# Kernel optimization log

Hardware: AMD Instinct MI355X
Metric: run time of the kernel (lower is better)

## Reference

```python
import jax, jax.numpy as jnp
import numpy as np

WS = 8       # window size
HEADS = 2    # num_heads hardcoded in CFPT's Swin_transformer blocks


def _to_windows(t, ws):
    # t: [B, H, W, C] -> [B*nWin, ws*ws, C]
    B, H, W, C = t.shape
    t = t.reshape(B, H // ws, ws, W // ws, ws, C)
    t = t.transpose(0, 1, 3, 2, 4, 5)
    return t.reshape(-1, ws * ws, C)


def _from_windows(t, B, H, W, ws):
    # t: [B*nWin, ws*ws, C] -> [B, H, W, C]
    C = t.shape[-1]
    t = t.reshape(B, H // ws, W // ws, ws, ws, C)
    t = t.transpose(0, 1, 3, 2, 4, 5)
    return t.reshape(B, H, W, C)


def swin_cross_attn(x, y, Wq, Wk, Wv, Wo):
    # Windowed cross-attention: queries from x, keys/values from y.
    # x, y: [B, C, H, W]; Wq/Wk/Wv/Wo: [C, C] (bias-free, no position embedding).
    B, C, H, W = x.shape
    dh = C // HEADS
    xw = _to_windows(x.transpose(0, 2, 3, 1), WS)   # [Bn, T, C], T = WS*WS
    yw = _to_windows(y.transpose(0, 2, 3, 1), WS)
    q = jnp.einsum('btc,dc->btd', xw, Wq)
    k = jnp.einsum('btc,dc->btd', yw, Wk)
    v = jnp.einsum('btc,dc->btd', yw, Wv)
    Bn, T, _ = q.shape
    q = q.reshape(Bn, T, HEADS, dh)
    k = k.reshape(Bn, T, HEADS, dh)
    v = v.reshape(Bn, T, HEADS, dh)
    scale = jnp.asarray(dh, x.dtype) ** -0.5
    scores = jnp.einsum('bqhd,bkhd->bhqk', q, k) * scale   # [Bn, H, T, T]
    attn = jax.nn.softmax(scores, axis=-1)
    o = jnp.einsum('bhqk,bkhd->bqhd', attn, v).reshape(Bn, T, C)
    o = jnp.einsum('btc,dc->btd', o, Wo)
    return _from_windows(o, B, H, W, WS).transpose(0, 3, 1, 2)  # [B, C, H, W]


def setup_inputs() -> dict:
    key = jax.random.key(0)
    ks = jax.random.split(key, 6)
    C = 256
    shapes = [(4, C, 128, 128), (4, C, 64, 64), (4, C, 32, 32), (4, C, 16, 16)]
    feats = [jax.random.normal(ks[i], s, jnp.float32) for i, s in enumerate(shapes)]
    w1 = jax.random.normal(ks[4], (4, 4, C, C), jnp.float32) * 0.02
    w2 = jax.random.normal(ks[5], (4, 4, C, C), jnp.float32) * 0.02
    return {"feat0": feats[0], "feat1": feats[1], "feat2": feats[2],
            "feat3": feats[3], "w1": w1, "w2": w2}


def reference(feat0, feat1, feat2, feat3, w1, w2):
    feats = [feat0, feat1, feat2, feat3]
    l = feats[0].shape[0] // 2
    outs = []
    for i, f in enumerate(feats):
        f1, f2 = f[:l], f[l:]
        # sequential cross-update, as in the original loop body
        f1 = jax.nn.relu(f1 + swin_cross_attn(f1, f2, w1[i, 0], w1[i, 1], w1[i, 2], w1[i, 3]))
        f2 = jax.nn.relu(f2 + swin_cross_attn(f2, f1, w2[i, 0], w2[i, 1], w2[i, 2], w2[i, 3]))
        outs.append(jnp.concatenate([f1, f2], axis=0))
    return tuple(outs)
```

## Files before the change

### kernel.cpp

```cpp
#include <hip/hip_runtime.h>


using bf16x8 = __attribute__((ext_vector_type(8))) __bf16;
using f32x4  = __attribute__((ext_vector_type(4))) float;
using u16x4  = __attribute__((ext_vector_type(4))) unsigned short;
using u16x8  = __attribute__((ext_vector_type(8))) unsigned short;

__device__ __forceinline__ unsigned short f2bf(float f){
  unsigned int x = __float_as_uint(f);
  x += 0x7FFFu + ((x >> 16) & 1u);
  return (unsigned short)(x >> 16);
}
__device__ __forceinline__ float bf2f(unsigned short u){
  return __uint_as_float((unsigned int)u << 16);
}
__device__ __forceinline__ void store_bf4(unsigned short* dst, f32x4 v){
  u16x4 o;
  o[0]=f2bf(v[0]); o[1]=f2bf(v[1]); o[2]=f2bf(v[2]); o[3]=f2bf(v[3]);
  *reinterpret_cast<u16x4*>(dst) = o;
}

#define MFMA16 __builtin_amdgcn_mfma_f32_16x16x32_bf16

__global__ void wcvt_kernel(const float* __restrict__ w1,
// ... 23 lines not shown
  int hw64 = (int)(HW >> 6);
  int bat = r / (4 * hw64);
  int r2 = r - bat * 4 * hw64;
  int ct = r2 / hw64, hwt = r2 - ct * hw64;

  const float* src = feat + (size_t)bat * HW * 256 + (size_t)(ct * 64) * HW + (size_t)hwt * 64;
  int tid = threadIdx.x;
  int cq = tid >> 4, hw0 = (tid & 15) * 4;
  #pragma unroll
  for (int p = 0; p < 4; ++p){
    int c = p * 16 + cq;
    const float* sp = src + (size_t)c * HW + hw0;
    float4 v = *reinterpret_cast<const float4*>(sp);
    T[c][hw0] = v.x; T[c][hw0+1] = v.y; T[c][hw0+2] = v.z; T[c][hw0+3] = v.w;
  }
  __syncthreads();
  unsigned short* dst = Ft + (tbase + (size_t)bat * HW + (size_t)hwt * 64) * 256 + ct * 64;
  #pragma unroll
  for (int p = 0; p < 2; ++p){
    int id = p * 256 + tid;
    int t = id >> 3, c0 = (id & 7) * 8;
    u16x8 o;
    #pragma unroll
    for (int j = 0; j < 8; ++j) o[j] = f2bf(T[c0 + j][t]);
    *reinterpret_cast<u16x8*>(dst + (size_t)t * 256 + c0) = o;
  }
}

__global__ __launch_bounds__(256, 2) void untrans_kernel(
    const unsigned short* __restrict__ Gt, float* __restrict__ outb)
{
  __shared__ float T[64][65];
  int bid = blockIdx.x;
  int r; int Hl; size_t tbase, ooff;
  if (bid < 4096){ r = bid;        Hl = 128; tbase = 0;     ooff = 0; }
  else if (bid < 5120){ r = bid - 4096; Hl = 64; tbase = 65536; ooff = 16777216; }
  else if (bid < 5376){ r = bid - 5120; Hl = 32; tbase = 81920; ooff = 20971520; }
  else { r = bid - 5376; Hl = 16; tbase = 86016; ooff = 22020096; }
  size_t HW = (size_t)Hl * Hl;
  int hw64 = (int)(HW >> 6);
  int bat = r / (4 * hw64);
  int r2 = r - bat * 4 * hw64;
  int ct = r2 / hw64, hwt = r2 - ct * hw64;

  const unsigned short* src = Gt + (tbase + (size_t)bat * HW + (size_t)hwt * 64) * 256 + ct * 64;
  int tid = threadIdx.x;
  #pragma unroll
  for (int p = 0; p < 2; ++p){
    int id = p * 256 + tid;
    int t = id >> 3, c0 = (id & 7) * 8;
    u16x8 v = *reinterpret_cast<const u16x8*>(src + (size_t)t * 256 + c0);
    #pragma unroll
    for (int j = 0; j < 8; ++j) T[t][c0 + j] = bf2f(v[j]);
  }
  __syncthreads();
  float* dst = outb + ooff + (size_t)bat * HW * 256 + (size_t)(ct * 64) * HW + (size_t)hwt * 64;
  int cq = tid >> 4, hw0 = (tid & 15) * 4;
  #pragma unroll
  for (int p = 0; p < 4; ++p){
    int c = p * 16 + cq;
    float4 v;
    v.x = T[hw0][c]; v.y = T[hw0+1][c]; v.z = T[hw0+2][c]; v.w = T[hw0+3][c];
    *reinterpret_cast<float4*>(dst + (size_t)c * HW + hw0) = v;
  }
}

struct WinGeo { int H, W, b, lvl; size_t HW, winoff, tbase, ooff; };

__device__ __forceinline__ WinGeo decode_win(int win){
  WinGeo g; int wloc;
  if (win < 512){ g.lvl = 0; wloc = win;      g.H = 128; g.tbase = 0;     g.ooff = 0; }
  else if (win < 640){ g.lvl = 1; wloc = win - 512; g.H = 64; g.tbase = 65536; g.ooff = 16777216; }
  else if (win < 672){ g.lvl = 2; wloc = win - 640; g.H = 32; g.tbase = 81920; g.ooff = 20971520; }
  else { g.lvl = 3; wloc = win - 672; g.H = 16; g.tbase = 86016; g.ooff = 22020096; }
  g.W = g.H; g.HW = (size_t)g.H * g.W;
  int nww = g.H >> 3, npb = nww * nww;
  g.b = wloc / npb;
  int r = wloc - g.b * npb;
  int wh = r / nww, ww = r - wh * nww;
  g.winoff = (size_t)(wh * 8) * g.W + (size_t)(ww * 8);
  return g;
}

__device__ __forceinline__ void flush_tile_td(const unsigned short* __restrict__ st,
    unsigned short* __restrict__ dst, int tid){
  #pragma unroll
  for (int p = 0; p < 8; ++p){
    int id = p * 256 + tid;
    int t = id >> 5, c = (id & 31) * 8;
    *reinterpret_cast<u16x8*>(dst + (size_t)t * 256 + c) =
      *reinterpret_cast<const u16x8*>(st + t * 264 + c);
  }
}
__device__ __forceinline__ void flush_tile_vt(const unsigned short* __restrict__ st,
    unsigned short* __restrict__ dst, int tid){
  #pragma unroll
  for (int p = 0; p < 8; ++p){
    int id = p * 256 + tid;
    int d = id >> 3, u = (id & 7) * 8;
    *reinterpret_cast<u16x8*>(dst + (size_t)d * 64 + u) =
      *reinterpret_cast<const u16x8*>(st + d * 72 + u);
  }
}

__global__ __launch_bounds__(256, 2) void proj_kernel(
    const unsigned short* __restrict__ Ft, const unsigned short* __restrict__ Gt,
    const unsigned short* __restrict__ wball,
    unsigned short* __restrict__ Qb, unsigned short* __restrict__ Kb,
    unsigned short* __restrict__ VTb, int phase)
{
  __shared__ alignas(16) unsigned short STK[64*264];
  __shared__ alignas(16) unsigned short STV[256*72];
  int win = blockIdx.x;
  WinGeo g = decode_win(win);
  int tid = threadIdx.x;
  int w = tid >> 6, l = tid & 63, l15 = l & 15, l4 = l >> 4, wd = w * 64;

  int batx = (phase == 0) ? g.b : g.b + 2;
  const unsigned short* Sx = Ft + (g.tbase + (size_t)batx * g.HW) * 256;
  const unsigned short* Sy = (phase == 0)
      ? Ft + (g.tbase + (size_t)(g.b + 2) * g.HW) * 256
      : Gt + (g.tbase + (size_t)g.b * g.HW) * 256;

  size_t rowo[4];
  #pragma unroll
  for (int ni = 0; ni < 4; ++ni){
    int t = ni * 16 + l15;
    rowo[ni] = ((size_t)g.winoff + (size_t)(t >> 3) * g.W + (t & 7)) * 256;
  }
  const unsigned short* Wbase = wball + ((size_t)(phase * 16 + g.lvl * 4) << 16);
  const unsigned short* Wq = Wbase;
  const unsigned short* Wk = Wbase + 65536;
  const unsigned short* Wv = Wbase + 131072;
  size_t woff = (size_t)win << 14;

  f32x4 ak[4][4], av[4][4];
  #pragma unroll
  for (int i = 0; i < 4; ++i)
    #pragma unroll
    for (int j = 0; j < 4; ++j){ ak[i][j] = f32x4{0.f,0.f,0.f,0.f}; av[i][j] = f32x4{0.f,0.f,0.f,0.f}; }
  #pragma unroll
  for (int ks = 0; ks < 8; ++ks){
    int k0 = ks * 32 + l4 * 8;
    bf16x8 tf[4], kf[4], vf[4];
    #pragma unroll
    for (int i = 0; i < 4; ++i){
      tf[i] = *reinterpret_cast<const bf16x8*>(Sy + rowo[i] + k0);
      kf[i] = *reinterpret_cast<const bf16x8*>(Wk + (size_t)((wd + i*16 + l15) * 256 + k0));
      vf[i] = *reinterpret_cast<const bf16x8*>(Wv + (size_t)((wd + i*16 + l15) * 256 + k0));
    }
    __builtin_amdgcn_s_setprio(1);
    #pragma unroll
    for (int mi = 0; mi < 4; ++mi)
      #pragma unroll
      for (int ni = 0; ni < 4; ++ni){
        ak[mi][ni] = MFMA16(kf[mi], tf[ni], ak[mi][ni], 0, 0, 0);
        av[mi][ni] = MFMA16(tf[mi], vf[ni], av[mi][ni], 0, 0, 0);
      }
    __builtin_amdgcn_s_setprio(0);
  }
  #pragma unroll
  for (int mi = 0; mi < 4; ++mi){
    int d0 = wd + mi*16 + l4*4;
    #pragma unroll
    for (int ni = 0; ni < 4; ++ni)
      store_bf4(&STK[(ni*16 + l15) * 264 + d0], ak[mi][ni]);
  }
  #pragma unroll
  for (int mi = 0; mi < 4; ++mi){
    int u0 = mi*16 + l4*4;
    #pragma unroll
    for (int ni = 0; ni < 4; ++ni)
      store_bf4(&STV[(wd + ni*16 + l15) * 72 + u0], av[mi][ni]);
  }
  __syncthreads();
  flush_tile_td(STK, Kb + woff, tid);
  flush_tile_vt(STV, VTb + woff, tid);

  f32x4 aq[4][4];
  #pragma unroll
  for (int i = 0; i < 4; ++i)
    #pragma unroll
    for (int j = 0; j < 4; ++j) aq[i][j] = f32x4{0.f,0.f,0.f,0.f};
  #pragma unroll
  for (int ks = 0; ks < 8; ++ks){
    int k0 = ks * 32 + l4 * 8;
    bf16x8 xf[4], qf[4];
    #pragma unroll
    for (int i = 0; i < 4; ++i){
      xf[i] = *reinterpret_cast<const bf16x8*>(Sx + rowo[i] + k0);
      qf[i] = *reinterpret_cast<const bf16x8*>(Wq + (size_t)((wd + i*16 + l15) * 256 + k0));
    }
    __builtin_amdgcn_s_setprio(1);
    #pragma unroll
    for (int mi = 0; mi < 4; ++mi)
      #pragma unroll
      for (int ni = 0; ni < 4; ++ni)
        aq[mi][ni] = MFMA16(qf[mi], xf[ni], aq[mi][ni], 0, 0, 0);
    __builtin_amdgcn_s_setprio(0);
  }
  __syncthreads();
  #pragma unroll
  for (int mi = 0; mi < 4; ++mi){
    int d0 = wd + mi*16 + l4*4;
    #pragma unroll
    for (int ni = 0; ni < 4; ++ni)
      store_bf4(&STK[(ni*16 + l15) * 264 + d0], aq[mi][ni]);
  }
  __syncthreads();
  flush_tile_td(STK, Qb + woff, tid);
}

__global__ __launch_bounds__(256, 3) void attnop_kernel(
    const unsigned short* __restrict__ Qb, const unsigned short* __restrict__ Kb,
    const unsigned short* __restrict__ VTb, const unsigned short* __restrict__ Ft,
    const unsigned short* __restrict__ wball,
    unsigned short* __restrict__ Gt, int phase)
{
  __shared__ alignas(16) unsigned short UB[64*264];
  int win = blockIdx.x;
  WinGeo g = decode_win(win);
  size_t woff = (size_t)win << 14;
  const unsigned short* Qw = Qb + woff;
  const unsigned short* Kw = Kb + woff;
  const unsigned short* VTw = VTb + woff;

  int tid = threadIdx.x;
  int w = tid >> 6, l = tid & 63, l15 = l & 15, l4 = l >> 4, wd = w * 64;
  int h = w >> 1, tc = w & 1;

  int bat = (phase == 0) ? g.b : g.b + 2;
  const unsigned short* Xres = Ft + (g.tbase + (size_t)bat * g.HW) * 256;
  unsigned short* Gout = Gt + (g.tbase + (size_t)bat * g.HW) * 256;
  const unsigned short* Wo = wball + ((size_t)(phase * 16 + g.lvl * 4 + 3) << 16);

  f32x4 s[4][2];
  #pragma unroll
  for (int i = 0; i < 4; ++i){ s[i][0] = f32x4{0.f,0.f,0.f,0.f}; s[i][1] = f32x4{0.f,0.f,0.f,0.f}; }
  #pragma unroll
  for (int ks = 0; ks < 4; ++ks){
    int k0 = h * 128 + ks * 32 + l4 * 8;
    bf16x8 a[4], bb[2];
    #pragma unroll
    for (int mi = 0; mi < 4; ++mi)
      a[mi] = *reinterpret_cast<const bf16x8*>(Kw + (size_t)(mi*16 + l15) * 256 + k0);
    #pragma unroll
    for (int ni = 0; ni < 2; ++ni)
      bb[ni] = *reinterpret_cast<const bf16x8*>(Qw + (size_t)(tc*32 + ni*16 + l15) * 256 + k0);
    __builtin_amdgcn_s_setprio(1);
    #pragma unroll
    for (int mi = 0; mi < 4; ++mi)
      #pragma unroll
      for (int ni = 0; ni < 2; ++ni)
        s[mi][ni] = MFMA16(a[mi], bb[ni], s[mi][ni], 0, 0, 0);
    __builtin_amdgcn_s_setprio(0);
  }

  const float SCL = 0.08838834764831845f;
  #pragma unroll
  for (int ni = 0; ni < 2; ++ni){
    float m = s[0][ni][0];
    #pragma unroll
    for (int mi = 0; mi < 4; ++mi)
      #pragma unroll
      for (int reg = 0; reg < 4; ++reg) m = fmaxf(m, s[mi][ni][reg]);
    m = fmaxf(m, __shfl_xor(m, 16));
    m = fmaxf(m, __shfl_xor(m, 32));
    float sum = 0.f;
    #pragma unroll
    for (int mi = 0; mi < 4; ++mi)
      #pragma unroll
      for (int reg = 0; reg < 4; ++reg){
        float e = __expf((s[mi][ni][reg] - m) * SCL);
        s[mi][ni][reg] = e; sum += e;
      }
    sum += __shfl_xor(sum, 16);
    sum += __shfl_xor(sum, 32);
    float rs = 1.0f / sum;
    int t = tc*32 + ni*16 + l15;
    #pragma unroll
    for (int mi = 0; mi < 4; ++mi){
      f32x4 pv;
      #pragma unroll
      for (int reg = 0; reg < 4; ++reg) pv[reg] = s[mi][ni][reg] * rs;
      store_bf4(&UB[h * 4608 + t * 72 + mi*16 + l4*4], pv);
    }
  }
  __syncthreads();

  f32x4 acc[4][4];
  #pragma unroll
  for (int i = 0; i < 4; ++i)
    #pragma unroll
    for (int j = 0; j < 4; ++j) acc[i][j] = f32x4{0.f,0.f,0.f,0.f};
  #pragma unroll
  for (int ks = 0; ks < 2; ++ks){
    int k0 = ks * 32 + l4 * 8;
    bf16x8 a[4], bb[4];
    #pragma unroll
    for (int mi = 0; mi < 4; ++mi)
      a[mi] = *reinterpret_cast<const bf16x8*>(VTw + (size_t)(wd + mi*16 + l15) * 64 + k0);
    #pragma unroll
    for (int ni = 0; ni < 4; ++ni)
      bb[ni] = *reinterpret_cast<const bf16x8*>(&UB[h * 4608 + (ni*16 + l15) * 72 + k0]);
    __builtin_amdgcn_s_setprio(1);
    #pragma unroll
    for (int mi = 0; mi < 4; ++mi)
      #pragma unroll
      for (int ni = 0; ni < 4; ++ni)
        acc[mi][ni] = MFMA16(a[mi], bb[ni], acc[mi][ni], 0, 0, 0);
    __builtin_amdgcn_s_setprio(0);
  }
  __syncthreads();
  #pragma unroll
  for (int mi = 0; mi < 4; ++mi){
    int c0 = wd + mi*16 + l4*4;
    #pragma unroll
    for (int ni = 0; ni < 4; ++ni)
      store_bf4(&UB[(ni*16 + l15) * 264 + c0], acc[mi][ni]);
  }
  __syncthreads();

  #pragma unroll
  for (int i = 0; i < 4; ++i)
    #pragma unroll
    for (int j = 0; j < 4; ++j) acc[i][j] = f32x4{0.f,0.f,0.f,0.f};
  #pragma unroll
  for (int ks = 0; ks < 8; ++ks){
    int k0 = ks * 32 + l4 * 8;
    bf16x8 a[4], bb[4];
    #pragma unroll
    for (int mi = 0; mi < 4; ++mi)
      a[mi] = *reinterpret_cast<const bf16x8*>(Wo + (size_t)((wd + mi*16 + l15) * 256 + k0));
    #pragma unroll
    for (int ni = 0; ni < 4; ++ni)
      bb[ni] = *reinterpret_cast<const bf16x8*>(&UB[(ni*16 + l15) * 264 + k0]);
    __builtin_amdgcn_s_setprio(1);
    #pragma unroll
    for (int mi = 0; mi < 4; ++mi)
      #pragma unroll
      for (int ni = 0; ni < 4; ++ni)
        acc[mi][ni] = MFMA16(a[mi], bb[ni], acc[mi][ni], 0, 0, 0);
    __builtin_amdgcn_s_setprio(0);
  }
  __syncthreads();
  #pragma unroll
  for (int mi = 0; mi < 4; ++mi){
    int c0 = wd + mi*16 + l4*4;
    #pragma unroll
    for (int ni = 0; ni < 4; ++ni)
      store_bf4(&UB[(ni*16 + l15) * 264 + c0], acc[mi][ni]);
  }
  __syncthreads();

  #pragma unroll
  for (int p = 0; p < 8; ++p){
    int id = p * 256 + tid;
    int t = id >> 5, c = (id & 31) * 8;
    size_t ro = ((size_t)g.winoff + (size_t)(t >> 3) * g.W + (t & 7)) * 256 + c;
    u16x8 ov = *reinterpret_cast<const u16x8*>(&UB[t * 264 + c]);
    u16x8 rv = *reinterpret_cast<const u16x8*>(Xres + ro);
    u16x8 o;
    #pragma unroll
    for (int j = 0; j < 8; ++j)
      o[j] = f2bf(fmaxf(bf2f(ov[j]) + bf2f(rv[j]), 0.f));
    *reinterpret_cast<u16x8*>(Gout + ro) = o;
  }
}

__global__ __launch_bounds__(256, 1) void swin_phase(
    const float* __restrict__ g0, const float* __restrict__ g1,
    const float* __restrict__ g2, const float* __restrict__ g3,
    const unsigned short* __restrict__ wball,
    float* __restrict__ outb, int phase)
{
  __shared__ alignas(16) unsigned short R0[64*264];
  __shared__ alignas(16) unsigned short R1[64*264];
  __shared__ alignas(16) unsigned short R2[256*72];
  __shared__ alignas(16) unsigned short R3[64*264];

  int bid = blockIdx.x;
  WinGeo g = decode_win(bid);
  const float* feat = (g.lvl == 0) ? g0 : (g.lvl == 1) ? g1 : (g.lvl == 2) ? g2 : g3;
  size_t CHW = g.HW * 256;

  const float* xsrc; const float* ysrc; float* outp;
  if (phase == 0){
    xsrc = feat + (size_t)g.b * CHW + g.winoff;
    ysrc = feat + (size_t)(g.b + 2) * CHW + g.winoff;
    outp = outb + g.ooff + (size_t)g.b * CHW + g.winoff;
  } else {
    xsrc = feat + (size_t)(g.b + 2) * CHW + g.winoff;
    ysrc = outb + g.ooff + (size_t)g.b * CHW + g.winoff;
    outp = outb + g.ooff + (size_t)(g.b + 2) * CHW + g.winoff;
  }
  const unsigned short* Wq = wball + ((size_t)(phase * 16 + g.lvl * 4) << 16);
  const unsigned short* Wk = Wq + 65536;
  const unsigned short* Wv = Wq + 2 * 65536;
  const unsigned short* Wo = Wq + 3 * 65536;

  int tid = threadIdx.x;
  int w = tid >> 6, l = tid & 63, l15 = l & 15, l4 = l >> 4, wd = w * 64;
  int hi0 = l >> 3, wi0 = l & 7;

  {
    const float* p0 = ysrc + (size_t)hi0 * g.W + wi0;
    #pragma unroll
    for (int oc = 0; oc < 8; ++oc){
      int c0 = (oc * 4 + w) * 8;
      const float* p = p0 + (size_t)c0 * g.HW;
      u16x8 uv;
      #pragma unroll
      for (int j = 0; j < 8; ++j) uv[j] = f2bf(p[(size_t)j * g.HW]);
      *reinterpret_cast<u16x8*>(&R0[l * 264 + c0]) = uv;
    }
  }
  __syncthreads();
  {
    f32x4 acc[4][4];
    #pragma unroll
    for (int i = 0; i < 4; ++i)
      #pragma unroll
      for (int j = 0; j < 4; ++j) acc[i][j] = f32x4{0.f,0.f,0.f,0.f};
    #pragma unroll
    for (int ks = 0; ks < 8; ++ks){
      int k0 = ks * 32 + l4 * 8;
      bf16x8 a[4], bb[4];
      #pragma unroll
      for (int mi = 0; mi < 4; ++mi)
        a[mi] = *reinterpret_cast<const bf16x8*>(Wk + (size_t)((wd + mi*16 + l15) * 256 + k0));
      #pragma unroll
      for (int ni = 0; ni < 4; ++ni)
        bb[ni] = *reinterpret_cast<const bf16x8*>(&R0[(ni*16 + l15) * 264 + k0]);
      #pragma unroll
      for (int mi = 0; mi < 4; ++mi)
        #pragma unroll
        for (int ni = 0; ni < 4; ++ni)
          acc[mi][ni] = MFMA16(a[mi], bb[ni], acc[mi][ni], 0, 0, 0);
    }
    #pragma unroll
    for (int mi = 0; mi < 4; ++mi){
      int d0 = wd + mi*16 + l4*4;
      #pragma unroll
      for (int ni = 0; ni < 4; ++ni)
// ... 138 lines not shown
    for (int i = 0; i < 4; ++i)
      #pragma unroll
      for (int j = 0; j < 4; ++j) acc[i][j] = f32x4{0.f,0.f,0.f,0.f};
    const unsigned short* P = R1;
    #pragma unroll
    for (int ks = 0; ks < 2; ++ks){
      int k0 = ks * 32 + l4 * 8;
      bf16x8 a[4], bb[4];
      #pragma unroll
      for (int mi = 0; mi < 4; ++mi)
        a[mi] = *reinterpret_cast<const bf16x8*>(&R2[(wdh + mi*16 + l15) * 72 + k0]);
      #pragma unroll
      for (int ni = 0; ni < 4; ++ni)
        bb[ni] = *reinterpret_cast<const bf16x8*>(&P[h * 4608 + (ni*16 + l15) * 72 + k0]);
      #pragma unroll
      for (int mi = 0; mi < 4; ++mi)
        #pragma unroll
        for (int ni = 0; ni < 4; ++ni)
          acc[mi][ni] = MFMA16(a[mi], bb[ni], acc[mi][ni], 0, 0, 0);
    }
    #pragma unroll
    for (int mi = 0; mi < 4; ++mi){
      int c0 = wdh + mi*16 + l4*4;
      #pragma unroll
      for (int ni = 0; ni < 4; ++ni)
        store_bf4(&R0[(ni*16 + l15) * 264 + c0], acc[mi][ni]);
    }
  }
  __syncthreads();
  {
    f32x4 acc[4][4];
    #pragma unroll
    for (int i = 0; i < 4; ++i)
      #pragma unroll
      for (int j = 0; j < 4; ++j) acc[i][j] = f32x4{0.f,0.f,0.f,0.f};
    #pragma unroll
    for (int ks = 0; ks < 8; ++ks){
      int k0 = ks * 32 + l4 * 8;
      bf16x8 a[4], bb[4];
      #pragma unroll
      for (int mi = 0; mi < 4; ++mi)
        a[mi] = *reinterpret_cast<const bf16x8*>(Wo + (size_t)((wd + mi*16 + l15) * 256 + k0));
      #pragma unroll
      for (int ni = 0; ni < 4; ++ni)
        bb[ni] = *reinterpret_cast<const bf16x8*>(&R0[(ni*16 + l15) * 264 + k0]);
      #pragma unroll
      for (int mi = 0; mi < 4; ++mi)
        #pragma unroll
        for (int ni = 0; ni < 4; ++ni)
          acc[mi][ni] = MFMA16(a[mi], bb[ni], acc[mi][ni], 0, 0, 0);
    }
    #pragma unroll
    for (int mi = 0; mi < 4; ++mi){
      #pragma unroll
      for (int ni = 0; ni < 4; ++ni){
        int t = ni*16 + l15, thi = t >> 3, twi = t & 7;
        size_t base = (size_t)(wd + mi*16 + l4*4) * g.HW + (size_t)thi * g.W + twi;
        #pragma unroll
        for (int reg = 0; reg < 4; ++reg){
          float res = xsrc[base + (size_t)reg * g.HW];
          float v = acc[mi][ni][reg] + res;
          outp[base + (size_t)reg * g.HW] = fmaxf(v, 0.f);
        }
      }
    }
  }
}

extern "C" void kernel_launch(void* const* d_in, const int* in_sizes, int n_in,
                              void* d_out, int out_size, void* d_ws, size_t ws_size,
                              hipStream_t stream) {
  (void)in_sizes; (void)n_in; (void)out_size;
  const float* f0 = (const float*)d_in[0];
  const float* f1 = (const float*)d_in[1];
  const float* f2 = (const float*)d_in[2];
  const float* f3 = (const float*)d_in[3];
  const float* w1 = (const float*)d_in[4];
  const float* w2 = (const float*)d_in[5];
  float* out = (float*)d_out;

  unsigned short* wbf = (unsigned short*)d_ws;
  const size_t WBF_B = 4194304;
  const size_t FT_B  = 44564480;
  const size_t QKV_B = 22282240;
  const size_t need  = WBF_B + 2 * FT_B + 3 * QKV_B;

  wcvt_kernel<<<2048, 256, 0, stream>>>(w1, w2, wbf);

  if (ws_size >= need){
    char* base = (char*)d_ws + WBF_B;
    unsigned short* Ft  = (unsigned short*)(base);
    unsigned short* Gt  = (unsigned short*)(base + FT_B);
    unsigned short* Qb  = (unsigned short*)(base + 2 * FT_B);
    unsigned short* Kb  = (unsigned short*)(base + 2 * FT_B + QKV_B);
    unsigned short* VTb = (unsigned short*)(base + 2 * FT_B + 2 * QKV_B);

    xpose_kernel<<<5440, 256, 0, stream>>>(f0, f1, f2, f3, Ft);
    for (int phase = 0; phase < 2; ++phase){
      proj_kernel<<<680, 256, 0, stream>>>(Ft, Gt, wbf, Qb, Kb, VTb, phase);
      attnop_kernel<<<680, 256, 0, stream>>>(Qb, Kb, VTb, Ft, wbf, Gt, phase);
    }
    untrans_kernel<<<5440, 256, 0, stream>>>(Gt, out);
  } else {
    swin_phase<<<680, 256, 0, stream>>>(f0, f1, f2, f3, wbf, out, 0);
    swin_phase<<<680, 256, 0, stream>>>(f0, f1, f2, f3, wbf, out, 1);
  }
}
```

Measured before the change: 237.7 us.

## Split QKV projection into three blocks per window for more parallelism

```diff
diff --git a/kernel.cpp b/kernel.cpp
--- a/kernel.cpp
+++ b/kernel.cpp
@@ -150,25 +150,27 @@
   }
 }
 
-__global__ __launch_bounds__(256, 2) void proj_kernel(
+__global__ __launch_bounds__(256, 4) void proj_kernel(
     const unsigned short* __restrict__ Ft, const unsigned short* __restrict__ Gt,
     const unsigned short* __restrict__ wball,
     unsigned short* __restrict__ Qb, unsigned short* __restrict__ Kb,
     unsigned short* __restrict__ VTb, int phase)
 {
-  __shared__ alignas(16) unsigned short STK[64*264];
-  __shared__ alignas(16) unsigned short STV[256*72];
-  int win = blockIdx.x;
+  __shared__ alignas(16) unsigned short ST[256*72];
+  int bid = blockIdx.x;
+  int win = bid / 3, ty = bid - win * 3;
   WinGeo g = decode_win(win);
   int tid = threadIdx.x;
   int w = tid >> 6, l = tid & 63, l15 = l & 15, l4 = l >> 4, wd = w * 64;
 
-  int batx = (phase == 0) ? g.b : g.b + 2;
-  const unsigned short* Sx = Ft + (g.tbase + (size_t)batx * g.HW) * 256;
-  const unsigned short* Sy = (phase == 0)
-      ? Ft + (g.tbase + (size_t)(g.b + 2) * g.HW) * 256
-      : Gt + (g.tbase + (size_t)g.b * g.HW) * 256;
-
+  const unsigned short* S;
+  if (ty == 2){
+    int batx = (phase == 0) ? g.b : g.b + 2;
+    S = Ft + (g.tbase + (size_t)batx * g.HW) * 256;
+  } else {
+    S = (phase == 0) ? Ft + (g.tbase + (size_t)(g.b + 2) * g.HW) * 256
+                     : Gt + (g.tbase + (size_t)g.b * g.HW) * 256;
+  }
   size_t rowo[4];
   #pragma unroll
   for (int ni = 0; ni < 4; ++ni){
@@ -176,86 +178,63 @@
     rowo[ni] = ((size_t)g.winoff + (size_t)(t >> 3) * g.W + (t & 7)) * 256;
   }
   const unsigned short* Wbase = wball + ((size_t)(phase * 16 + g.lvl * 4) << 16);
-  const unsigned short* Wq = Wbase;
-  const unsigned short* Wk = Wbase + 65536;
-  const unsigned short* Wv = Wbase + 131072;
+  const unsigned short* Wm = (ty == 0) ? Wbase + 65536
+                           : (ty == 1) ? Wbase + 131072 : Wbase;
   size_t woff = (size_t)win << 14;
 
-  f32x4 ak[4][4], av[4][4];
+  f32x4 acc[4][4];
   #pragma unroll
   for (int i = 0; i < 4; ++i)
     #pragma unroll
-    for (int j = 0; j < 4; ++j){ ak[i][j] = f32x4{0.f,0.f,0.f,0.f}; av[i][j] = f32x4{0.f,0.f,0.f,0.f}; }
+    for (int j = 0; j < 4; ++j) acc[i][j] = f32x4{0.f,0.f,0.f,0.f};
+
   #pragma unroll
   for (int ks = 0; ks < 8; ++ks){
     int k0 = ks * 32 + l4 * 8;
-    bf16x8 tf[4], kf[4], vf[4];
+    bf16x8 tf[4], wf[4];
     #pragma unroll
     for (int i = 0; i < 4; ++i){
-      tf[i] = *reinterpret_cast<const bf16x8*>(Sy + rowo[i] + k0);
-      kf[i] = *reinterpret_cast<const bf16x8*>(Wk + (size_t)((wd + i*16 + l15) * 256 + k0));
-      vf[i] = *reinterpret_cast<const bf16x8*>(Wv + (size_t)((wd + i*16 + l15) * 256 + k0));
+      tf[i] = *reinterpret_cast<const bf16x8*>(S + rowo[i] + k0);
+      wf[i] = *reinterpret_cast<const bf16x8*>(Wm + (size_t)((wd + i*16 + l15) * 256 + k0));
     }
     __builtin_amdgcn_s_setprio(1);
-    #pragma unroll
-    for (int mi = 0; mi < 4; ++mi)
-      #pragma unroll
-      for (int ni = 0; ni < 4; ++ni){
-        ak[mi][ni] = MFMA16(kf[mi], tf[ni], ak[mi][ni], 0, 0, 0);
-        av[mi][ni] = MFMA16(tf[mi], vf[ni], av[mi][ni], 0, 0, 0);
-      }
+    if (ty == 1){
+      #pragma unroll
+      for (int mi = 0; mi < 4; ++mi)
+        #pragma unroll
+        for (int ni = 0; ni < 4; ++ni)
+          acc[mi][ni] = MFMA16(tf[mi], wf[ni], acc[mi][ni], 0, 0, 0);
+    } else {
+      #pragma unroll
+      for (int mi = 0; mi < 4; ++mi)
+        #pragma unroll
+        for (int ni = 0; ni < 4; ++ni)
+          acc[mi][ni] = MFMA16(wf[mi], tf[ni], acc[mi][ni], 0, 0, 0);
+    }
     __builtin_amdgcn_s_setprio(0);
   }
-  #pragma unroll
-  for (int mi = 0; mi < 4; ++mi){
-    int d0 = wd + mi*16 + l4*4;
-    #pragma unroll
-    for (int ni = 0; ni < 4; ++ni)
-      store_bf4(&STK[(ni*16 + l15) * 264 + d0], ak[mi][ni]);
-  }
-  #pragma unroll
-  for (int mi = 0; mi < 4; ++mi){
-    int u0 = mi*16 + l4*4;
-    #pragma unroll
-    for (int ni = 0; ni < 4; ++ni)
-      store_bf4(&STV[(wd + ni*16 + l15) * 72 + u0], av[mi][ni]);
-  }
-  __syncthreads();
-  flush_tile_td(STK, Kb + woff, tid);
-  flush_tile_vt(STV, VTb + woff, tid);
-
-  f32x4 aq[4][4];
-  #pragma unroll
-  for (int i = 0; i < 4; ++i)
-    #pragma unroll
-    for (int j = 0; j < 4; ++j) aq[i][j] = f32x4{0.f,0.f,0.f,0.f};
-  #pragma unroll
-  for (int ks = 0; ks < 8; ++ks){
-    int k0 = ks * 32 + l4 * 8;
-    bf16x8 xf[4], qf[4];
-    #pragma unroll
-    for (int i = 0; i < 4; ++i){
-      xf[i] = *reinterpret_cast<const bf16x8*>(Sx + rowo[i] + k0);
-      qf[i] = *reinterpret_cast<const bf16x8*>(Wq + (size_t)((wd + i*16 + l15) * 256 + k0));
-    }
-    __builtin_amdgcn_s_setprio(1);
-    #pragma unroll
-    for (int mi = 0; mi < 4; ++mi)
-      #pragma unroll
-      for (int ni = 0; ni < 4; ++ni)
-        aq[mi][ni] = MFMA16(qf[mi], xf[ni], aq[mi][ni], 0, 0, 0);
-    __builtin_amdgcn_s_setprio(0);
-  }
-  __syncthreads();
-  #pragma unroll
-  for (int mi = 0; mi < 4; ++mi){
-    int d0 = wd + mi*16 + l4*4;
-    #pragma unroll
-    for (int ni = 0; ni < 4; ++ni)
-      store_bf4(&STK[(ni*16 + l15) * 264 + d0], aq[mi][ni]);
-  }
-  __syncthreads();
-  flush_tile_td(STK, Qb + woff, tid);
+
+  if (ty == 1){
+    #pragma unroll
+    for (int mi = 0; mi < 4; ++mi){
+      int u0 = mi*16 + l4*4;
+      #pragma unroll
+      for (int ni = 0; ni < 4; ++ni)
+        store_bf4(&ST[(wd + ni*16 + l15) * 72 + u0], acc[mi][ni]);
+    }
+    __syncthreads();
+    flush_tile_vt(ST, VTb + woff, tid);
+  } else {
+    #pragma unroll
+    for (int mi = 0; mi < 4; ++mi){
+      int d0 = wd + mi*16 + l4*4;
+      #pragma unroll
+      for (int ni = 0; ni < 4; ++ni)
+        store_bf4(&ST[(ni*16 + l15) * 264 + d0], acc[mi][ni]);
+    }
+    __syncthreads();
+    flush_tile_td(ST, ((ty == 0) ? Kb : Qb) + woff, tid);
+  }
 }
 
 __global__ __launch_bounds__(256, 3) void attnop_kernel(
@@ -726,7 +705,7 @@
 
     xpose_kernel<<<5440, 256, 0, stream>>>(f0, f1, f2, f3, Ft);
     for (int phase = 0; phase < 2; ++phase){
-      proj_kernel<<<680, 256, 0, stream>>>(Ft, Gt, wbf, Qb, Kb, VTb, phase);
+      proj_kernel<<<2040, 256, 0, stream>>>(Ft, Gt, wbf, Qb, Kb, VTb, phase);
       attnop_kernel<<<680, 256, 0, stream>>>(Qb, Kb, VTb, Ft, wbf, Gt, phase);
     }
     untrans_kernel<<<5440, 256, 0, stream>>>(Gt, out);
```

Result: slower. 426.1 us (+79.3%).

## Split fused K/V projection into separate passes to raise proj kernel occupancy

Applied to the files above, without the earlier changes.

```diff
diff --git a/kernel.cpp b/kernel.cpp
--- a/kernel.cpp
+++ b/kernel.cpp
@@ -150,14 +150,13 @@
   }
 }
 
-__global__ __launch_bounds__(256, 2) void proj_kernel(
+__global__ __launch_bounds__(256, 4) void proj_kernel(
     const unsigned short* __restrict__ Ft, const unsigned short* __restrict__ Gt,
     const unsigned short* __restrict__ wball,
     unsigned short* __restrict__ Qb, unsigned short* __restrict__ Kb,
     unsigned short* __restrict__ VTb, int phase)
 {
-  __shared__ alignas(16) unsigned short STK[64*264];
-  __shared__ alignas(16) unsigned short STV[256*72];
+  __shared__ alignas(16) unsigned short ST[256*72];
   int win = blockIdx.x;
   WinGeo g = decode_win(win);
   int tid = threadIdx.x;
@@ -181,81 +180,109 @@
   const unsigned short* Wv = Wbase + 131072;
   size_t woff = (size_t)win << 14;
 
-  f32x4 ak[4][4], av[4][4];
-  #pragma unroll
-  for (int i = 0; i < 4; ++i)
-    #pragma unroll
-    for (int j = 0; j < 4; ++j){ ak[i][j] = f32x4{0.f,0.f,0.f,0.f}; av[i][j] = f32x4{0.f,0.f,0.f,0.f}; }
-  #pragma unroll
-  for (int ks = 0; ks < 8; ++ks){
-    int k0 = ks * 32 + l4 * 8;
-    bf16x8 tf[4], kf[4], vf[4];
-    #pragma unroll
-    for (int i = 0; i < 4; ++i){
-      tf[i] = *reinterpret_cast<const bf16x8*>(Sy + rowo[i] + k0);
-      kf[i] = *reinterpret_cast<const bf16x8*>(Wk + (size_t)((wd + i*16 + l15) * 256 + k0));
-      vf[i] = *reinterpret_cast<const bf16x8*>(Wv + (size_t)((wd + i*16 + l15) * 256 + k0));
-    }
-    __builtin_amdgcn_s_setprio(1);
-    #pragma unroll
-    for (int mi = 0; mi < 4; ++mi)
-      #pragma unroll
-      for (int ni = 0; ni < 4; ++ni){
-        ak[mi][ni] = MFMA16(kf[mi], tf[ni], ak[mi][ni], 0, 0, 0);
-        av[mi][ni] = MFMA16(tf[mi], vf[ni], av[mi][ni], 0, 0, 0);
+  {
+    f32x4 acc[4][4];
+    #pragma unroll
+    for (int i = 0; i < 4; ++i)
+      #pragma unroll
+      for (int j = 0; j < 4; ++j) acc[i][j] = f32x4{0.f,0.f,0.f,0.f};
+    #pragma unroll
+    for (int ks = 0; ks < 8; ++ks){
+      int k0 = ks * 32 + l4 * 8;
+      bf16x8 tf[4], wf[4];
+      #pragma unroll
+      for (int i = 0; i < 4; ++i){
+        tf[i] = *reinterpret_cast<const bf16x8*>(Sy + rowo[i] + k0);
+        wf[i] = *reinterpret_cast<const bf16x8*>(Wk + (size_t)((wd + i*16 + l15) * 256 + k0));
       }
-    __builtin_amdgcn_s_setprio(0);
-  }
-  #pragma unroll
-  for (int mi = 0; mi < 4; ++mi){
-    int d0 = wd + mi*16 + l4*4;
-    #pragma unroll
-    for (int ni = 0; ni < 4; ++ni)
-      store_bf4(&STK[(ni*16 + l15) * 264 + d0], ak[mi][ni]);
-  }
-  #pragma unroll
-  for (int mi = 0; mi < 4; ++mi){
-    int u0 = mi*16 + l4*4;
-    #pragma unroll
-    for (int ni = 0; ni < 4; ++ni)
-      store_bf4(&STV[(wd + ni*16 + l15) * 72 + u0], av[mi][ni]);
-  }
-  __syncthreads();
-  flush_tile_td(STK, Kb + woff, tid);
-  flush_tile_vt(STV, VTb + woff, tid);
-
-  f32x4 aq[4][4];
-  #pragma unroll
-  for (int i = 0; i < 4; ++i)
-    #pragma unroll
-    for (int j = 0; j < 4; ++j) aq[i][j] = f32x4{0.f,0.f,0.f,0.f};
-  #pragma unroll
-  for (int ks = 0; ks < 8; ++ks){
-    int k0 = ks * 32 + l4 * 8;
-    bf16x8 xf[4], qf[4];
-    #pragma unroll
-    for (int i = 0; i < 4; ++i){
-      xf[i] = *reinterpret_cast<const bf16x8*>(Sx + rowo[i] + k0);
-      qf[i] = *reinterpret_cast<const bf16x8*>(Wq + (size_t)((wd + i*16 + l15) * 256 + k0));
-    }
-    __builtin_amdgcn_s_setprio(1);
-    #pragma unroll
-    for (int mi = 0; mi < 4; ++mi)
-      #pragma unroll
-      for (int ni = 0; ni < 4; ++ni)
-        aq[mi][ni] = MFMA16(qf[mi], xf[ni], aq[mi][ni], 0, 0, 0);
-    __builtin_amdgcn_s_setprio(0);
-  }
-  __syncthreads();
-  #pragma unroll
-  for (int mi = 0; mi < 4; ++mi){
-    int d0 = wd + mi*16 + l4*4;
-    #pragma unroll
-    for (int ni = 0; ni < 4; ++ni)
-      store_bf4(&STK[(ni*16 + l15) * 264 + d0], aq[mi][ni]);
-  }
-  __syncthreads();
-  flush_tile_td(STK, Qb + woff, tid);
+      __builtin_amdgcn_s_setprio(1);
+      #pragma unroll
+      for (int mi = 0; mi < 4; ++mi)
+        #pragma unroll
+        for (int ni = 0; ni < 4; ++ni)
+          acc[mi][ni] = MFMA16(wf[mi], tf[ni], acc[mi][ni], 0, 0, 0);
+      __builtin_amdgcn_s_setprio(0);
+    }
+    #pragma unroll
+    for (int mi = 0; mi < 4; ++mi){
+      int d0 = wd + mi*16 + l4*4;
+      #pragma unroll
+      for (int ni = 0; ni < 4; ++ni)
+        store_bf4(&ST[(ni*16 + l15) * 264 + d0], acc[mi][ni]);
+    }
+    __syncthreads();
+    flush_tile_td(ST, Kb + woff, tid);
+  }
+
+  {
+    f32x4 acc[4][4];
+    #pragma unroll
+    for (int i = 0; i < 4; ++i)
+      #pragma unroll
+      for (int j = 0; j < 4; ++j) acc[i][j] = f32x4{0.f,0.f,0.f,0.f};
+    #pragma unroll
+    for (int ks = 0; ks < 8; ++ks){
+      int k0 = ks * 32 + l4 * 8;
+      bf16x8 tf[4], wf[4];
+      #pragma unroll
+      for (int i = 0; i < 4; ++i){
+        tf[i] = *reinterpret_cast<const bf16x8*>(Sy + rowo[i] + k0);
+        wf[i] = *reinterpret_cast<const bf16x8*>(Wv + (size_t)((wd + i*16 + l15) * 256 + k0));
+      }
+      __builtin_amdgcn_s_setprio(1);
+      #pragma unroll
+      for (int mi = 0; mi < 4; ++mi)
+        #pragma unroll
+        for (int ni = 0; ni < 4; ++ni)
+          acc[mi][ni] = MFMA16(tf[mi], wf[ni], acc[mi][ni], 0, 0, 0);
+      __builtin_amdgcn_s_setprio(0);
+    }
+    __syncthreads();
+    #pragma unroll
+    for (int mi = 0; mi < 4; ++mi){
+      int u0 = mi*16 + l4*4;
+      #pragma unroll
+      for (int ni = 0; ni < 4; ++ni)
+        store_bf4(&ST[(wd + ni*16 + l15) * 72 + u0], acc[mi][ni]);
+    }
+    __syncthreads();
+    flush_tile_vt(ST, VTb + woff, tid);
+  }
+
+  {
+    f32x4 acc[4][4];
+    #pragma unroll
+    for (int i = 0; i < 4; ++i)
+      #pragma unroll
+      for (int j = 0; j < 4; ++j) acc[i][j] = f32x4{0.f,0.f,0.f,0.f};
+    #pragma unroll
+    for (int ks = 0; ks < 8; ++ks){
+      int k0 = ks * 32 + l4 * 8;
+      bf16x8 tf[4], wf[4];
+      #pragma unroll
+      for (int i = 0; i < 4; ++i){
+        tf[i] = *reinterpret_cast<const bf16x8*>(Sx + rowo[i] + k0);
+        wf[i] = *reinterpret_cast<const bf16x8*>(Wq + (size_t)((wd + i*16 + l15) * 256 + k0));
+      }
+      __builtin_amdgcn_s_setprio(1);
+      #pragma unroll
+      for (int mi = 0; mi < 4; ++mi)
+        #pragma unroll
+        for (int ni = 0; ni < 4; ++ni)
+          acc[mi][ni] = MFMA16(wf[mi], tf[ni], acc[mi][ni], 0, 0, 0);
+      __builtin_amdgcn_s_setprio(0);
+    }
+    __syncthreads();
+    #pragma unroll
+    for (int mi = 0; mi < 4; ++mi){
+      int d0 = wd + mi*16 + l4*4;
+      #pragma unroll
+      for (int ni = 0; ni < 4; ++ni)
+        store_bf4(&ST[(ni*16 + l15) * 264 + d0], acc[mi][ni]);
+    }
+    __syncthreads();
+    flush_tile_td(ST, Qb + woff, tid);
+  }
 }
 
 __global__ __launch_bounds__(256, 3) void attnop_kernel(
```

After: 272.9 us. +14.8%, slower.

## Fuse QKV projection and attention kernels into one per-window kernel

Applied to the files above, without the earlier changes.

```diff
diff --git a/kernel.cpp b/kernel.cpp
--- a/kernel.cpp
+++ b/kernel.cpp
@@ -129,45 +129,25 @@
   return g;
 }
 
-__device__ __forceinline__ void flush_tile_td(const unsigned short* __restrict__ st,
-    unsigned short* __restrict__ dst, int tid){
-  #pragma unroll
-  for (int p = 0; p < 8; ++p){
-    int id = p * 256 + tid;
-    int t = id >> 5, c = (id & 31) * 8;
-    *reinterpret_cast<u16x8*>(dst + (size_t)t * 256 + c) =
-      *reinterpret_cast<const u16x8*>(st + t * 264 + c);
-  }
-}
-__device__ __forceinline__ void flush_tile_vt(const unsigned short* __restrict__ st,
-    unsigned short* __restrict__ dst, int tid){
-  #pragma unroll
-  for (int p = 0; p < 8; ++p){
-    int id = p * 256 + tid;
-    int d = id >> 3, u = (id & 7) * 8;
-    *reinterpret_cast<u16x8*>(dst + (size_t)d * 64 + u) =
-      *reinterpret_cast<const u16x8*>(st + d * 72 + u);
-  }
-}
-
-__global__ __launch_bounds__(256, 2) void proj_kernel(
-    const unsigned short* __restrict__ Ft, const unsigned short* __restrict__ Gt,
+__global__ __launch_bounds__(256, 2) void swin_win(
+    const unsigned short* __restrict__ Ft, const unsigned short* __restrict__ Gtin,
     const unsigned short* __restrict__ wball,
-    unsigned short* __restrict__ Qb, unsigned short* __restrict__ Kb,
-    unsigned short* __restrict__ VTb, int phase)
+    unsigned short* __restrict__ Gt, int phase)
 {
-  __shared__ alignas(16) unsigned short STK[64*264];
-  __shared__ alignas(16) unsigned short STV[256*72];
+  __shared__ alignas(16) unsigned short A[64*264];
+  __shared__ alignas(16) unsigned short B[256*72];
   int win = blockIdx.x;
   WinGeo g = decode_win(win);
   int tid = threadIdx.x;
   int w = tid >> 6, l = tid & 63, l15 = l & 15, l4 = l >> 4, wd = w * 64;
+  int h = w >> 1, tc = w & 1;
 
   int batx = (phase == 0) ? g.b : g.b + 2;
   const unsigned short* Sx = Ft + (g.tbase + (size_t)batx * g.HW) * 256;
   const unsigned short* Sy = (phase == 0)
       ? Ft + (g.tbase + (size_t)(g.b + 2) * g.HW) * 256
-      : Gt + (g.tbase + (size_t)g.b * g.HW) * 256;
+      : Gtin + (g.tbase + (size_t)g.b * g.HW) * 256;
+  unsigned short* Gout = Gt + (g.tbase + (size_t)batx * g.HW) * 256;
 
   size_t rowo[4];
   #pragma unroll
@@ -179,107 +159,76 @@
   const unsigned short* Wq = Wbase;
   const unsigned short* Wk = Wbase + 65536;
   const unsigned short* Wv = Wbase + 131072;
-  size_t woff = (size_t)win << 14;
-
-  f32x4 ak[4][4], av[4][4];
-  #pragma unroll
-  for (int i = 0; i < 4; ++i)
-    #pragma unroll
-    for (int j = 0; j < 4; ++j){ ak[i][j] = f32x4{0.f,0.f,0.f,0.f}; av[i][j] = f32x4{0.f,0.f,0.f,0.f}; }
-  #pragma unroll
-  for (int ks = 0; ks < 8; ++ks){
-    int k0 = ks * 32 + l4 * 8;
-    bf16x8 tf[4], kf[4], vf[4];
-    #pragma unroll
-    for (int i = 0; i < 4; ++i){
-      tf[i] = *reinterpret_cast<const bf16x8*>(Sy + rowo[i] + k0);
-      kf[i] = *reinterpret_cast<const bf16x8*>(Wk + (size_t)((wd + i*16 + l15) * 256 + k0));
-      vf[i] = *reinterpret_cast<const bf16x8*>(Wv + (size_t)((wd + i*16 + l15) * 256 + k0));
-    }
-    __builtin_amdgcn_s_setprio(1);
-    #pragma unroll
-    for (int mi = 0; mi < 4; ++mi)
-      #pragma unroll
-      for (int ni = 0; ni < 4; ++ni){
-        ak[mi][ni] = MFMA16(kf[mi], tf[ni], ak[mi][ni], 0, 0, 0);
-        av[mi][ni] = MFMA16(tf[mi], vf[ni], av[mi][ni], 0, 0, 0);
+  const unsigned short* Wo = Wbase + 196608;
+
+  f32x4 av[4][4];
+  {
+    f32x4 ak[4][4];
+    #pragma unroll
+    for (int i = 0; i < 4; ++i)
+      #pragma unroll
+      for (int j = 0; j < 4; ++j){ ak[i][j] = f32x4{0.f,0.f,0.f,0.f}; av[i][j] = f32x4{0.f,0.f,0.f,0.f}; }
+    #pragma unroll
+    for (int ks = 0; ks < 8; ++ks){
+      int k0 = ks * 32 + l4 * 8;
+      bf16x8 tf[4], kf[4], vf[4];
+      #pragma unroll
+      for (int i = 0; i < 4; ++i){
+        tf[i] = *reinterpret_cast<const bf16x8*>(Sy + rowo[i] + k0);
+        kf[i] = *reinterpret_cast<const bf16x8*>(Wk + (size_t)((wd + i*16 + l15) * 256 + k0));
+        vf[i] = *reinterpret_cast<const bf16x8*>(Wv + (size_t)((wd + i*16 + l15) * 256 + k0));
       }
-    __builtin_amdgcn_s_setprio(0);
-  }
-  #pragma unroll
-  for (int mi = 0; mi < 4; ++mi){
-    int d0 = wd + mi*16 + l4*4;
-    #pragma unroll
-    for (int ni = 0; ni < 4; ++ni)
-      store_bf4(&STK[(ni*16 + l15) * 264 + d0], ak[mi][ni]);
-  }
-  #pragma unroll
-  for (int mi = 0; mi < 4; ++mi){
-    int u0 = mi*16 + l4*4;
-    #pragma unroll
-    for (int ni = 0; ni < 4; ++ni)
-      store_bf4(&STV[(wd + ni*16 + l15) * 72 + u0], av[mi][ni]);
-  }
-  __syncthreads();
-  flush_tile_td(STK, Kb + woff, tid);
-  flush_tile_vt(STV, VTb + woff, tid);
-
-  f32x4 aq[4][4];
-  #pragma unroll
-  for (int i = 0; i < 4; ++i)
-    #pragma unroll
-    for (int j = 0; j < 4; ++j) aq[i][j] = f32x4{0.f,0.f,0.f,0.f};
-  #pragma unroll
-  for (int ks = 0; ks < 8; ++ks){
-    int k0 = ks * 32 + l4 * 8;
-    bf16x8 xf[4], qf[4];
-    #pragma unroll
-    for (int i = 0; i < 4; ++i){
-      xf[i] = *reinterpret_cast<const bf16x8*>(Sx + rowo[i] + k0);
-      qf[i] = *reinterpret_cast<const bf16x8*>(Wq + (size_t)((wd + i*16 + l15) * 256 + k0));
-    }
-    __builtin_amdgcn_s_setprio(1);
-    #pragma unroll
-    for (int mi = 0; mi < 4; ++mi)
-      #pragma unroll
-      for (int ni = 0; ni < 4; ++ni)
-        aq[mi][ni] = MFMA16(qf[mi], xf[ni], aq[mi][ni], 0, 0, 0);
-    __builtin_amdgcn_s_setprio(0);
-  }
-  __syncthreads();
-  #pragma unroll
-  for (int mi = 0; mi < 4; ++mi){
-    int d0 = wd + mi*16 + l4*4;
-    #pragma unroll
-    for (int ni = 0; ni < 4; ++ni)
-      store_bf4(&STK[(ni*16 + l15) * 264 + d0], aq[mi][ni]);
-  }
-  __syncthreads();
-  flush_tile_td(STK, Qb + woff, tid);
-}
-
-__global__ __launch_bounds__(256, 3) void attnop_kernel(
-    const unsigned short* __restrict__ Qb, const unsigned short* __restrict__ Kb,
-    const unsigned short* __restrict__ VTb, const unsigned short* __restrict__ Ft,
-    const unsigned short* __restrict__ wball,
-    unsigned short* __restrict__ Gt, int phase)
-{
-  __shared__ alignas(16) unsigned short UB[64*264];
-  int win = blockIdx.x;
-  WinGeo g = decode_win(win);
-  size_t woff = (size_t)win << 14;
-  const unsigned short* Qw = Qb + woff;
-  const unsigned short* Kw = Kb + woff;
-  const unsigned short* VTw = VTb + woff;
-
-  int tid = threadIdx.x;
-  int w = tid >> 6, l = tid & 63, l15 = l & 15, l4 = l >> 4, wd = w * 64;
-  int h = w >> 1, tc = w & 1;
-
-  int bat = (phase == 0) ? g.b : g.b + 2;
-  const unsigned short* Xres = Ft + (g.tbase + (size_t)bat * g.HW) * 256;
-  unsigned short* Gout = Gt + (g.tbase + (size_t)bat * g.HW) * 256;
-  const unsigned short* Wo = wball + ((size_t)(phase * 16 + g.lvl * 4 + 3) << 16);
+      __builtin_amdgcn_s_setprio(1);
+      #pragma unroll
+      for (int mi = 0; mi < 4; ++mi)
+        #pragma unroll
+        for (int ni = 0; ni < 4; ++ni){
+          ak[mi][ni] = MFMA16(kf[mi], tf[ni], ak[mi][ni], 0, 0, 0);
+          av[mi][ni] = MFMA16(tf[mi], vf[ni], av[mi][ni], 0, 0, 0);
+        }
+      __builtin_amdgcn_s_setprio(0);
+    }
+    #pragma unroll
+    for (int mi = 0; mi < 4; ++mi){
+      int d0 = wd + mi*16 + l4*4;
+      #pragma unroll
+      for (int ni = 0; ni < 4; ++ni)
+        store_bf4(&A[(ni*16 + l15) * 264 + d0], ak[mi][ni]);
+    }
+  }
+
+  {
+    f32x4 aq[4][4];
+    #pragma unroll
+    for (int i = 0; i < 4; ++i)
+      #pragma unroll
+      for (int j = 0; j < 4; ++j) aq[i][j] = f32x4{0.f,0.f,0.f,0.f};
+    #pragma unroll
+    for (int ks = 0; ks < 8; ++ks){
+      int k0 = ks * 32 + l4 * 8;
+      bf16x8 tf[4], wf[4];
+      #pragma unroll
+      for (int i = 0; i < 4; ++i){
+        tf[i] = *reinterpret_cast<const bf16x8*>(Sx + rowo[i] + k0);
+        wf[i] = *reinterpret_cast<const bf16x8*>(Wq + (size_t)((wd + i*16 + l15) * 256 + k0));
+      }
+      __builtin_amdgcn_s_setprio(1);
+      #pragma unroll
+      for (int mi = 0; mi < 4; ++mi)
+        #pragma unroll
+        for (int ni = 0; ni < 4; ++ni)
+          aq[mi][ni] = MFMA16(wf[mi], tf[ni], aq[mi][ni], 0, 0, 0);
+      __builtin_amdgcn_s_setprio(0);
+    }
+    #pragma unroll
+    for (int mi = 0; mi < 4; ++mi){
+      int d0 = wd + mi*16 + l4*4;
+      #pragma unroll
+      for (int ni = 0; ni < 4; ++ni)
+        store_bf4(&B[(ni*16 + l15) * 264 + d0], aq[mi][ni]);
+    }
+  }
+  __syncthreads();
 
   f32x4 s[4][2];
   #pragma unroll
@@ -290,10 +239,10 @@
     bf16x8 a[4], bb[2];
     #pragma unroll
     for (int mi = 0; mi < 4; ++mi)
-      a[mi] = *reinterpret_cast<const bf16x8*>(Kw + (size_t)(mi*16 + l15) * 256 + k0);
+      a[mi] = *reinterpret_cast<const bf16x8*>(&A[(mi*16 + l15) * 264 + k0]);
     #pragma unroll
     for (int ni = 0; ni < 2; ++ni)
-      bb[ni] = *reinterpret_cast<const bf16x8*>(Qw + (size_t)(tc*32 + ni*16 + l15) * 256 + k0);
+      bb[ni] = *reinterpret_cast<const bf16x8*>(&B[(tc*32 + ni*16 + l15) * 264 + k0]);
     __builtin_amdgcn_s_setprio(1);
     #pragma unroll
     for (int mi = 0; mi < 4; ++mi)
@@ -301,6 +250,15 @@
       for (int ni = 0; ni < 2; ++ni)
         s[mi][ni] = MFMA16(a[mi], bb[ni], s[mi][ni], 0, 0, 0);
     __builtin_amdgcn_s_setprio(0);
+  }
+  __syncthreads();
+
+  #pragma unroll
+  for (int mi = 0; mi < 4; ++mi){
+    int u0 = mi*16 + l4*4;
+    #pragma unroll
+    for (int ni = 0; ni < 4; ++ni)
+      store_bf4(&B[(wd + ni*16 + l15) * 72 + u0], av[mi][ni]);
   }
 
   const float SCL = 0.08838834764831845f;
@@ -330,7 +288,7 @@
       f32x4 pv;
       #pragma unroll
       for (int reg = 0; reg < 4; ++reg) pv[reg] = s[mi][ni][reg] * rs;
-      store_bf4(&UB[h * 4608 + t * 72 + mi*16 + l4*4], pv);
+      store_bf4(&A[h * 4608 + t * 72 + mi*16 + l4*4], pv);
     }
   }
   __syncthreads();
@@ -346,10 +304,10 @@
     bf16x8 a[4], bb[4];
     #pragma unroll
     for (int mi = 0; mi < 4; ++mi)
-      a[mi] = *reinterpret_cast<const bf16x8*>(VTw + (size_t)(wd + mi*16 + l15) * 64 + k0);
+      a[mi] = *reinterpret_cast<const bf16x8*>(&B[(wd + mi*16 + l15) * 72 + k0]);
     #pragma unroll
     for (int ni = 0; ni < 4; ++ni)
-      bb[ni] = *reinterpret_cast<const bf16x8*>(&UB[h * 4608 + (ni*16 + l15) * 72 + k0]);
+      bb[ni] = *reinterpret_cast<const bf16x8*>(&A[h * 4608 + (ni*16 + l15) * 72 + k0]);
     __builtin_amdgcn_s_setprio(1);
     #pragma unroll
     for (int mi = 0; mi < 4; ++mi)
@@ -364,7 +322,7 @@
     int c0 = wd + mi*16 + l4*4;
     #pragma unroll
     for (int ni = 0; ni < 4; ++ni)
-      store_bf4(&UB[(ni*16 + l15) * 264 + c0], acc[mi][ni]);
+      store_bf4(&A[(ni*16 + l15) * 264 + c0], acc[mi][ni]);
   }
   __syncthreads();
 
@@ -381,7 +339,7 @@
       a[mi] = *reinterpret_cast<const bf16x8*>(Wo + (size_t)((wd + mi*16 + l15) * 256 + k0));
     #pragma unroll
     for (int ni = 0; ni < 4; ++ni)
-      bb[ni] = *reinterpret_cast<const bf16x8*>(&UB[(ni*16 + l15) * 264 + k0]);
+      bb[ni] = *reinterpret_cast<const bf16x8*>(&A[(ni*16 + l15) * 264 + k0]);
     __builtin_amdgcn_s_setprio(1);
     #pragma unroll
     for (int mi = 0; mi < 4; ++mi)
@@ -396,7 +354,7 @@
     int c0 = wd + mi*16 + l4*4;
     #pragma unroll
     for (int ni = 0; ni < 4; ++ni)
-      store_bf4(&UB[(ni*16 + l15) * 264 + c0], acc[mi][ni]);
+      store_bf4(&A[(ni*16 + l15) * 264 + c0], acc[mi][ni]);
   }
   __syncthreads();
 
@@ -405,8 +363,8 @@
     int id = p * 256 + tid;
     int t = id >> 5, c = (id & 31) * 8;
     size_t ro = ((size_t)g.winoff + (size_t)(t >> 3) * g.W + (t & 7)) * 256 + c;
-    u16x8 ov = *reinterpret_cast<const u16x8*>(&UB[t * 264 + c]);
-    u16x8 rv = *reinterpret_cast<const u16x8*>(Xres + ro);
+    u16x8 ov = *reinterpret_cast<const u16x8*>(&A[t * 264 + c]);
+    u16x8 rv = *reinterpret_cast<const u16x8*>(Sx + ro);
     u16x8 o;
     #pragma unroll
     for (int j = 0; j < 8; ++j)
@@ -711,24 +669,18 @@
   unsigned short* wbf = (unsigned short*)d_ws;
   const size_t WBF_B = 4194304;
   const size_t FT_B  = 44564480;
-  const size_t QKV_B = 22282240;
-  const size_t need  = WBF_B + 2 * FT_B + 3 * QKV_B;
+  const size_t need  = WBF_B + 2 * FT_B;
 
   wcvt_kernel<<<2048, 256, 0, stream>>>(w1, w2, wbf);
 
   if (ws_size >= need){
     char* base = (char*)d_ws + WBF_B;
-    unsigned short* Ft  = (unsigned short*)(base);
-    unsigned short* Gt  = (unsigned short*)(base + FT_B);
-    unsigned short* Qb  = (unsigned short*)(base + 2 * FT_B);
-    unsigned short* Kb  = (unsigned short*)(base + 2 * FT_B + QKV_B);
-    unsigned short* VTb = (unsigned short*)(base + 2 * FT_B + 2 * QKV_B);
+    unsigned short* Ft = (unsigned short*)(base);
+    unsigned short* Gt = (unsigned short*)(base + FT_B);
 
     xpose_kernel<<<5440, 256, 0, stream>>>(f0, f1, f2, f3, Ft);
-    for (int phase = 0; phase < 2; ++phase){
-      proj_kernel<<<680, 256, 0, stream>>>(Ft, Gt, wbf, Qb, Kb, VTb, phase);
-      attnop_kernel<<<680, 256, 0, stream>>>(Qb, Kb, VTb, Ft, wbf, Gt, phase);
-    }
+    for (int phase = 0; phase < 2; ++phase)
+      swin_win<<<680, 256, 0, stream>>>(Ft, Gt, wbf, Gt, phase);
     untrans_kernel<<<5440, 256, 0, stream>>>(Gt, out);
   } else {
     swin_phase<<<680, 256, 0, stream>>>(f0, f1, f2, f3, wbf, out, 0);
```

After: 198.9 us (median of 2 runs). -16.3%, faster.
